# Kernel optimization log

Measured on AMD Instinct MI355X. Metric: run time of the kernel, lower is better.

The kernel has to match this reference:

```python
import jax, jax.numpy as jnp
import numpy as np

EPS = 1e-8
K_KNN = 20

def vn_lin(W, x):
    # W: [Cout, Cin], x: [B, Cin, 3, ...] -> [B, Cout, 3, ...]
    return jnp.einsum('oi,bi...->bo...', W, x)

def vn_relu(Wd, x):
    # VNLeakyReLU with negative_slope=0, share_nonlinearity=False
    d = jnp.einsum('oi,bi...->bo...', Wd, x)
    dot = jnp.sum(x * d, axis=2, keepdims=True)   # sum over 3-vector axis
    dsq = jnp.sum(d * d, axis=2, keepdims=True) + EPS
    return jnp.where(dot >= 0, x, x - (dot / dsq) * d)

def graph_feature_cross(p, k):
    # p: [B, N, 3] -> feat: [B, 3, 3, N, k]
    xx = jnp.sum(p * p, axis=-1)                       # [B,N]
    inner = jnp.einsum('bnd,bmd->bnm', p, p)           # [B,N,N]
    neg_dist = 2.0 * inner - xx[:, :, None] - xx[:, None, :]
    idx = jax.lax.top_k(neg_dist, k)[1]                # [B,N,k] nearest neighbors
    nbrs = jax.vmap(lambda pb, ib: pb[ib])(p, idx)     # [B,N,k,3]
    xr = jnp.broadcast_to(p[:, :, None, :], nbrs.shape)
    cross = jnp.cross(nbrs, xr)                        # [B,N,k,3]
    feat = jnp.stack([nbrs - xr, xr, cross], axis=3)   # [B,N,k,3(ch),3(vec)]
    return jnp.transpose(feat, (0, 3, 4, 1, 2))        # [B,3,3,N,k]

def setup_inputs() -> dict:
    key = jax.random.key(0)
    ks = jax.random.split(key, 9)
    B, N = 4, 2048
    H = 128           # hidden_dim // 3
    C_IN = 2 * H      # 256
    CC = 128          # c_dim // 3
    s_in = 1.0 / np.sqrt(C_IN)
    s_h = 1.0 / np.sqrt(H)
    return {
        'p': jax.random.normal(ks[0], (B, N, 3), dtype=jnp.float32),
        'fc_pos_W': jax.random.normal(ks[1], (C_IN, 3), dtype=jnp.float32) / np.sqrt(3.0),
        'blk_d0': jax.random.normal(ks[2], (5, C_IN, C_IN), dtype=jnp.float32) * s_in,
        'blk_W0': jax.random.normal(ks[3], (5, H, C_IN), dtype=jnp.float32) * s_in,
        'blk_d1': jax.random.normal(ks[4], (5, H, H), dtype=jnp.float32) * s_h,
        'blk_W1': jax.random.normal(ks[5], (5, H, H), dtype=jnp.float32) * s_h,
        'blk_Ws': jax.random.normal(ks[6], (5, H, C_IN), dtype=jnp.float32) * s_in,
        'fc_c_W': jax.random.normal(ks[7], (CC, H), dtype=jnp.float32) * s_h,
        'act_d': jax.random.normal(ks[8], (H, H), dtype=jnp.float32) * s_h,
    }

def reference(p, fc_pos_W, blk_d0, blk_W0, blk_d1, blk_W1, blk_Ws, fc_c_W, act_d):
    feat = graph_feature_cross(p, K_KNN)          # [B,3,3,N,k]
    x = vn_lin(fc_pos_W, feat)                    # [B,256,3,N,k]
    net = jnp.mean(x, axis=-1)                    # mean_pool over k -> [B,256,3,N]

    def block(i, x):
        h = vn_lin(blk_W0[i], vn_relu(blk_d0[i], x))
        dx = vn_lin(blk_W1[i], vn_relu(blk_d1[i], h))
        return vn_lin(blk_Ws[i], x) + dx          # shortcut (size_in != size_out)

    net = block(0, net)                           # [B,128,3,N]
    for i in range(1, 5):
        pooled = jnp.broadcast_to(jnp.mean(net, axis=3, keepdims=True), net.shape)
        net = block(i, jnp.concatenate([net, pooled], axis=1))
    net = jnp.mean(net, axis=3)                   # [B,128,3]
    c = vn_lin(fc_c_W, vn_relu(act_d, net))       # [B,128,3]
    return c.reshape(c.shape[0], -1)              # [B,384]
```

## Files before the change

### kernel.cpp

```cpp
#include <hip/hip_runtime.h>
#include <math.h>

#define N_PTS 2048
#define K_NN  20
#define K_D   10
#define WTOT  819200

typedef unsigned short u16;
typedef unsigned int   u32;
typedef _Float16 f16;
using half8   = __attribute__((ext_vector_type(8))) _Float16;
using floatx4 = __attribute__((ext_vector_type(4))) float;

__device__ __forceinline__ void split2h(float v, f16& h, f16& l) {
    h = (f16)v;
    l = (f16)((v - (float)h) * 1024.0f);
}

__device__ __forceinline__ float neg_dist(float4 q2, float4 c) {
    return fmaf(q2.x, c.x, fmaf(q2.y, c.y, fmaf(q2.z, c.z, -q2.w))) - c.w;
}

__global__ __launch_bounds__(256) void prep_kernel(
    const float* __restrict__ pts, float* __restrict__ m_out,
    const float* __restrict__ bd0, const float* __restrict__ bW0,
    const float* __restrict__ bd1, const float* __restrict__ bW1,
    const float* __restrict__ bWs, u16* __restrict__ Wswz,
    float* __restrict__ nm_acc)
{
    __shared__ float4 sp[N_PTS];
    if (blockIdx.x >= 1024) {
        int i = (blockIdx.x - 1024) * 256 + threadIdx.x;
        if (i >= WTOT) return;
        if (i < 7680) nm_acc[i] = 0.f;
        float v; int base, K, local;
        if (i < 327680)      { int rel = i;          base = (rel/65536)*65536;            local = rel%65536; K = 256; v = bd0[rel]; }
        else if (i < 491520) { int rel = i - 327680; base = 327680 + (rel/32768)*32768;   local = rel%32768; K = 256; v = bW0[rel]; }
        else if (i < 573440) { int rel = i - 491520; base = 491520 + (rel/16384)*16384;   local = rel%16384; K = 128; v = bd1[rel]; }
        else if (i < 655360) { int rel = i - 573440; base = 573440 + (rel/16384)*16384;   local = rel%16384; K = 128; v = bW1[rel]; }
        else                 { int rel = i - 655360; base = 655360 + (rel/32768)*32768;   local = rel%32768; K = 256; v = bWs[rel]; }
        int m = local / K, k = local % K;
        int NKF = K >> 5;
        int mf = m >> 4, r = m & 15;
        int kf = k >> 5, q = (k >> 3) & 3, ii = k & 7;
        int lane = q*16 + r;
        int dst = base + ((mf*NKF + kf)*64 + lane)*8 + ii;
        f16 h, l; split2h(v, h, l);
        f16* W = (f16*)Wswz;
        W[dst] = h; W[WTOT + dst] = l;
        return;
    }

    const int b     = blockIdx.x >> 8;
    const int qbase = (blockIdx.x & 255) << 3;
    const int ql    = threadIdx.x >> 5;
    const int sl    = threadIdx.x & 31;
    const float* pb = pts + (size_t)b * N_PTS * 3;
    for (int i = threadIdx.x; i < N_PTS; i += 256) {
        float x = pb[i*3+0], y = pb[i*3+1], z = pb[i*3+2];
        sp[i] = make_float4(x, y, z, x*x + y*y + z*z);
    }
    __syncthreads();

    const int n = qbase + ql;
    const float4 q = sp[n];
    const float4 q2 = make_float4(2.f*q.x, 2.f*q.y, 2.f*q.z, q.w);

    float t[K_D];
#pragma unroll
    for (int s = 0; s < K_D; ++s) t[s] = -INFINITY;

    for (int j = 0; j < N_PTS/32; ++j) {
        float4 c = sp[j*32 + sl];
        float v = neg_dist(q2, c);
#pragma unroll
        for (int s = 0; s < K_D; ++s) {
            float nx = (s < K_D-1) ? t[s+1] : INFINITY;
            t[s] = fminf(fmaxf(t[s], v), nx);
        }
    }

    float head = t[K_D-1];
    float T = -INFINITY;
#pragma unroll 1
    for (int e = 0; e < K_NN; ++e) {
        float v = head; int w = sl;
#pragma unroll
        for (int off = 1; off < 32; off <<= 1) {
            float vo = __shfl_xor(v, off);
            int   wo = __shfl_xor(w, off);
            bool take = (vo > v) || (vo == v && wo < w);
            v = take ? vo : v;
            w = take ? wo : w;
        }
        T = v;
        if (w == sl) {
#pragma unroll
            for (int s = K_D-1; s > 0; --s) t[s] = t[s-1];
            t[0] = -INFINITY;
            head = t[K_D-1];
        }
    }

    float sx = 0.f, sy = 0.f, sz = 0.f;
    for (int j = 0; j < N_PTS/32; ++j) {
        float4 c = sp[j*32 + sl];
        float v = neg_dist(q2, c);
        if (v >= T) { sx += c.x; sy += c.y; sz += c.z; }
    }
#pragma unroll
    for (int off = 1; off < 32; off <<= 1) {
        sx += __shfl_xor(sx, off);
        sy += __shfl_xor(sy, off);
        sz += __shfl_xor(sz, off);
    }
    if (sl == 0) {
        const float inv = 1.0f / (float)K_NN;
        const int pt = b * N_PTS + n;
        m_out[pt*3+0] = sx * inv;
        m_out[pt*3+1] = sy * inv;
        m_out[pt*3+2] = sz * inv;
    }
}

template<int MF, int JF>
__device__ __forceinline__ void run_gemm_hi(
    const f16* __restrict__ Whi, size_t aoff,
    int NK, const f16* Blds, int bstride, int lane,
    floatx4 (&acc)[MF][JF])
{
    const int l15 = lane & 15;
    const int lq8 = (lane >> 4) * 8;
    half8 Aa[MF], Ab[MF];

    auto loada = [&](half8 (&dst)[MF], int kf) {
#pragma unroll
        for (int fm = 0; fm < MF; ++fm)
            dst[fm] = *(const half8*)(Whi + aoff + (size_t)(fm*NK + kf)*512 + (size_t)lane*8);
    };
    auto step = [&](half8 (&af)[MF], int kf) {
        half8 bq[JF];
#pragma unroll
        for (int fj = 0; fj < JF; ++fj)
            bq[fj] = *(const half8*)&Blds[(fj*16 + l15)*bstride + kf*32 + lq8];
#pragma unroll
        for (int fm = 0; fm < MF; ++fm)
#pragma unroll
            for (int fj = 0; fj < JF; ++fj)
                acc[fm][fj] = __builtin_amdgcn_mfma_f32_16x16x32_f16(af[fm], bq[fj], acc[fm][fj], 0, 0, 0);
    };

    loada(Aa, 0);
#pragma unroll 1
    for (int kf = 0; kf < NK; kf += 2) {
        loada(Ab, kf + 1);
        step(Aa, kf);
        if (kf + 2 < NK) loada(Aa, kf + 2);
        step(Ab, kf + 1);
    }
}

template<int MF, int JF>
__device__ __forceinline__ void run_gemm_split(
    const f16* __restrict__ Whi, const f16* __restrict__ Wlo, size_t aoff,
    int NK, const f16* Blds, int bstride, int lane,
    floatx4 (&acc)[MF][JF], floatx4 (&accL)[MF][JF])
{
    const int l15 = lane & 15;
    const int lq8 = (lane >> 4) * 8;
    half8 Aa[2*MF], Ab[2*MF];

    auto loada = [&](half8 (&dst)[2*MF], int kf) {
#pragma unroll
        for (int fm = 0; fm < MF; ++fm) {
            size_t fo = aoff + (size_t)(fm*NK + kf)*512 + (size_t)lane*8;
            dst[fm*2+0] = *(const half8*)(Whi + fo);
            dst[fm*2+1] = *(const half8*)(Wlo + fo);
        }
    };
    auto step = [&](half8 (&af)[2*MF], int kf) {
        half8 bq[JF];
#pragma unroll
        for (int fj = 0; fj < JF; ++fj)
            bq[fj] = *(const half8*)&Blds[(fj*16 + l15)*bstride + kf*32 + lq8];
#pragma unroll
        for (int fm = 0; fm < MF; ++fm)
#pragma unroll
            for (int fj = 0; fj < JF; ++fj) {
                acc[fm][fj]  = __builtin_amdgcn_mfma_f32_16x16x32_f16(af[fm*2+0], bq[fj], acc[fm][fj], 0, 0, 0);
                accL[fm][fj] = __builtin_amdgcn_mfma_f32_16x16x32_f16(af[fm*2+1], bq[fj], accL[fm][fj], 0, 0, 0);
            }
    };

    loada(Aa, 0);
#pragma unroll 1
    for (int kf = 0; kf < NK; kf += 2) {
        loada(Ab, kf + 1);
        step(Aa, kf);
        if (kf + 2 < NK) loada(Aa, kf + 2);
        step(Ab, kf + 1);
    }
}

__device__ __forceinline__ uint2 pack_res(floatx4 a, floatx4 aL) {
    u16 hh[4];
#pragma unroll
    for (int r = 0; r < 4; ++r) {
        f16 hv = (f16)(a[r] + aL[r] * (1.0f/1024.0f));
        hh[r] = *(u16*)&hv;
    }
    uint2 pv;
    pv.x = (u32)hh[0] | ((u32)hh[1] << 16);
    pv.y = (u32)hh[2] | ((u32)hh[3] << 16);
    return pv;
}

__device__ __forceinline__ uint2 pack_hi(floatx4 a) {
    u16 hh[4];
#pragma unroll
    for (int r = 0; r < 4; ++r) {
        f16 hv = (f16)a[r];
        hh[r] = *(u16*)&hv;
    }
    uint2 pv;
    pv.x = (u32)hh[0] | ((u32)hh[1] << 16);
    pv.y = (u32)hh[2] | ((u32)hh[3] << 16);
    return pv;
}

__global__ __launch_bounds__(256, 3) void resblk_kernel(
    const u16* __restrict__ Wswz,
    int offD0, int offW0, int offD1, int offW1, int offWs,
    const f16* __restrict__ netIn, const float* __restrict__ nm_prev,
    const float* __restrict__ pts, const float* __restrict__ m_buf,
    const float* __restrict__ fcW,
    f16* __restrict__ netOut, float* __restrict__ nm_out, int blk0,
    int skip_store)
{
    __shared__ struct {
        f16 X[48*264];
        union { f16 d[48*264]; float C[48*132]; } Y;
    } s;

    const int tid  = threadIdx.x;
    const int jb   = blockIdx.x * 48;
    const int bB   = blockIdx.x >> 7;
    const int lane = tid & 63;
    const int wv   = tid >> 6;
    const f16* Whi = (const f16*)Wswz;
    const f16* Wlo = Whi + WTOT;

    if (blk0) {
        float* Hf = (float*)s.Y.C;
        const int ptbase = blockIdx.x * 16;
        for (int i = tid; i < 768; i += 256) Hf[i] = fcW[i];
        if (tid < 96) Hf[768 + tid] = (tid < 48) ? pts[ptbase*3 + tid]
                                                 : m_buf[ptbase*3 + tid - 48];
        __syncthreads();
#pragma unroll 1
        for (int it = 0; it < 6; ++it) {
            int idx = tid + 256*it;
            int r = idx >> 5;
            int cg = idx & 31;
            int l = r / 3, v = r - l*3;
            float pv0[3] = {Hf[768+l*3], Hf[768+l*3+1], Hf[768+l*3+2]};
            float mv0[3] = {Hf[816+l*3], Hf[816+l*3+1], Hf[816+l*3+2]};
            int v1 = (v==2) ? 0 : v+1;
            int v2 = (v==0) ? 2 : v-1;
            float av = mv0[v] - pv0[v];
            float bv = pv0[v];
            float cv = mv0[v1]*pv0[v2] - mv0[v2]*pv0[v1];
            half8 o;
#pragma unroll
            for (int k = 0; k < 8; ++k) {
                int ch = cg*8 + k;
                o[k] = (f16)(Hf[ch*3+0]*av + Hf[ch*3+1]*bv + Hf[ch*3+2]*cv);
            }
            *(half8*)&s.X[r*264 + cg*8] = o;
        }
    } else {
#pragma unroll 1
        for (int it = 0; it < 6; ++it) {
            int idx = tid + 256*it;
            int r = idx >> 5;
            int cg = idx & 31;
            if (cg < 16) {
                uint4 vv = *(const uint4*)(netIn + (size_t)(jb + r)*128 + cg*8);
                *(uint4*)&s.X[r*264 + cg*8] = vv;
            } else {
                int v = r % 3;
                const float* np = nm_prev + (bB*3+v)*128 + (cg-16)*8;
                half8 o;
#pragma unroll
                for (int k = 0; k < 8; ++k) o[k] = (f16)(np[k] * (1.0f/2048.0f));
                *(half8*)&s.X[r*264 + cg*8] = o;
            }
        }
    }
    __syncthreads();

    floatx4 acc4[2][3], accL4[2][3];
#pragma unroll
    for (int a = 0; a < 2; ++a)
#pragma unroll
        for (int b = 0; b < 3; ++b) { acc4[a][b] = (floatx4){0,0,0,0}; accL4[a][b] = (floatx4){0,0,0,0}; }

    {
        floatx4 acc[4][3];
#pragma unroll
        for (int a = 0; a < 4; ++a)
#pragma unroll
            for (int b = 0; b < 3; ++b) acc[a][b] = (floatx4){0,0,0,0};
        run_gemm_hi<4,3>(Whi, (size_t)offD0 + (size_t)wv*16384, 8, s.X, 264, lane, acc);
#pragma unroll
        for (int fm = 0; fm < 4; ++fm)
#pragma unroll
            for (int fj = 0; fj < 3; ++fj) {
                int mloc = wv*64 + fm*16 + (lane>>4)*4;
                int jl   = fj*16 + (lane & 15);
                *(uint2*)&s.Y.d[jl*264 + mloc] = pack_hi(acc[fm][fj]);
            }
    }
    __syncthreads();

    run_gemm_split<2,3>(Whi, Wlo, (size_t)offWs + (size_t)wv*8192, 8, s.X, 264, lane, acc4, accL4);

#pragma unroll 1
    for (int it = 0; it < 2; ++it) {
        int idx = tid + 256*it;
        int l = idx >> 5, cg = idx & 31;
        half8 xa = *(const half8*)&s.X[(l*3+0)*264 + cg*8];
        half8 xb = *(const half8*)&s.X[(l*3+1)*264 + cg*8];
        half8 xc = *(const half8*)&s.X[(l*3+2)*264 + cg*8];
        half8 da = *(const half8*)&s.Y.d[(l*3+0)*264 + cg*8];
        half8 db = *(const half8*)&s.Y.d[(l*3+1)*264 + cg*8];
        half8 dc = *(const half8*)&s.Y.d[(l*3+2)*264 + cg*8];
        half8 ya, yb, yc;
#pragma unroll
        for (int k = 0; k < 8; ++k) {
            float x0 = (float)xa[k], x1 = (float)xb[k], x2 = (float)xc[k];
            float d0 = (float)da[k], d1 = (float)db[k], d2 = (float)dc[k];
            float dot = x0*d0 + x1*d1 + x2*d2;
            float y0, y1, y2;
            if (dot >= 0.f) { y0 = x0; y1 = x1; y2 = x2; }
            else {
                float dsq = d0*d0 + d1*d1 + d2*d2 + 1e-8f;
                float sc = dot / dsq;
                y0 = x0 - sc*d0; y1 = x1 - sc*d1; y2 = x2 - sc*d2;
            }
            ya[k] = (f16)y0; yb[k] = (f16)y1; yc[k] = (f16)y2;
        }
        *(half8*)&s.Y.d[(l*3+0)*264 + cg*8] = ya;
        *(half8*)&s.Y.d[(l*3+1)*264 + cg*8] = yb;
        *(half8*)&s.Y.d[(l*3+2)*264 + cg*8] = yc;
    }
    __syncthreads();

    {
        floatx4 acc[2][3], accL[2][3];
#pragma unroll
        for (int a = 0; a < 2; ++a)
#pragma unroll
            for (int b = 0; b < 3; ++b) { acc[a][b] = (floatx4){0,0,0,0}; accL[a][b] = (floatx4){0,0,0,0}; }
        run_gemm_split<2,3>(Whi, Wlo, (size_t)offW0 + (size_t)wv*8192, 8, s.Y.d, 264, lane, acc, accL);
#pragma unroll
        for (int fm = 0; fm < 2; ++fm)
#pragma unroll
            for (int fj = 0; fj < 3; ++fj) {
                int mloc = wv*32 + fm*16 + (lane>>4)*4;
                int jl   = fj*16 + (lane & 15);
                *(uint2*)&s.X[jl*136 + mloc] = pack_res(acc[fm][fj], accL[fm][fj]);
            }
    }
    __syncthreads();

    {
        floatx4 acc[2][3];
#pragma unroll
        for (int a = 0; a < 2; ++a)
#pragma unroll
            for (int b = 0; b < 3; ++b) acc[a][b] = (floatx4){0,0,0,0};
        run_gemm_hi<2,3>(Whi, (size_t)offD1 + (size_t)wv*4096, 4, s.X, 136, lane, acc);
#pragma unroll
        for (int fm = 0; fm < 2; ++fm)
#pragma unroll
            for (int fj = 0; fj < 3; ++fj) {
                int mloc = wv*32 + fm*16 + (lane>>4)*4;
                int jl   = fj*16 + (lane & 15);
                *(uint2*)&s.Y.d[jl*136 + mloc] = pack_hi(acc[fm][fj]);
            }
    }
    __syncthreads();

    {
        int l = tid >> 4, cg = tid & 15;
        half8 xa = *(const half8*)&s.X[(l*3+0)*136 + cg*8];
        half8 xb = *(const half8*)&s.X[(l*3+1)*136 + cg*8];
        half8 xc = *(const half8*)&s.X[(l*3+2)*136 + cg*8];
        half8 da = *(const half8*)&s.Y.d[(l*3+0)*136 + cg*8];
        half8 db = *(const half8*)&s.Y.d[(l*3+1)*136 + cg*8];
        half8 dc = *(const half8*)&s.Y.d[(l*3+2)*136 + cg*8];
        half8 ya, yb, yc;
#pragma unroll
        for (int k = 0; k < 8; ++k) {
            float x0 = (float)xa[k], x1 = (float)xb[k], x2 = (float)xc[k];
            float d0 = (float)da[k], d1 = (float)db[k], d2 = (float)dc[k];
            float dot = x0*d0 + x1*d1 + x2*d2;
            float y0, y1, y2;
            if (dot >= 0.f) { y0 = x0; y1 = x1; y2 = x2; }
            else {
                float dsq = d0*d0 + d1*d1 + d2*d2 + 1e-8f;
                float sc = dot / dsq;
                y0 = x0 - sc*d0; y1 = x1 - sc*d1; y2 = x2 - sc*d2;
            }
            ya[k] = (f16)y0; yb[k] = (f16)y1; yc[k] = (f16)y2;
        }
        __syncthreads();
        *(half8*)&s.X[(l*3+0)*136 + cg*8] = ya;
        *(half8*)&s.X[(l*3+1)*136 + cg*8] = yb;
        *(half8*)&s.X[(l*3+2)*136 + cg*8] = yc;
    }
    __syncthreads();

    run_gemm_split<2,3>(Whi, Wlo, (size_t)offW1 + (size_t)wv*4096, 4, s.X, 136, lane, acc4, accL4);

#pragma unroll
    for (int fm = 0; fm < 2; ++fm)
#pragma unroll
        for (int fj = 0; fj < 3; ++fj) {
            int mloc = wv*32 + fm*16 + (lane>>4)*4;
            int jl   = fj*16 + (lane & 15);
            floatx4 res;
#pragma unroll
            for (int r = 0; r < 4; ++r) res[r] = acc4[fm][fj][r] + accL4[fm][fj][r] * (1.0f/1024.0f);
            if (!skip_store) {
                u16 hh[4];
#pragma unroll
                for (int r = 0; r < 4; ++r) { f16 hv = (f16)res[r]; hh[r] = *(u16*)&hv; }
                uint2 pv;
                pv.x = (u32)hh[0] | ((u32)hh[1] << 16);
                pv.y = (u32)hh[2] | ((u32)hh[3] << 16);
                *(uint2*)(netOut + (size_t)(jb + jl)*128 + mloc) = pv;
            }
            *(floatx4*)&s.Y.C[jl*132 + mloc] = res;
        }
    __syncthreads();

#pragma unroll 1
    for (int idx = tid; idx < 384; idx += 256) {
        int v = idx >> 7, ch = idx & 127;
        float sum = 0.f;
#pragma unroll 1
        for (int pt = 0; pt < 16; ++pt) sum += s.Y.C[(pt*3+v)*132 + ch];
        atomicAdd(nm_out + (bB*3+v)*128 + ch, sum);
    }
}

__global__ __launch_bounds__(128) void final_kernel(const float* __restrict__ nm_sum,
                                                    const float* __restrict__ act_d,
                                                    const float* __restrict__ fc_c,
                                                    float* __restrict__ out)
{
    const int b = blockIdx.x;
    const int c = threadIdx.x;
    __shared__ float xs[128][3];
    __shared__ float ys[128][3];
    xs[c][0] = nm_sum[(b*3+0)*128 + c] * (1.0f/2048.0f);
    xs[c][1] = nm_sum[(b*3+1)*128 + c] * (1.0f/2048.0f);
    xs[c][2] = nm_sum[(b*3+2)*128 + c] * (1.0f/2048.0f);
    __syncthreads();
    float d0 = 0.f, d1 = 0.f, d2 = 0.f;
    for (int i = 0; i < 128; ++i) {
        float w = act_d[c*128 + i];
        d0 = fmaf(w, xs[i][0], d0);
        d1 = fmaf(w, xs[i][1], d1);
        d2 = fmaf(w, xs[i][2], d2);
    }
    float x0 = xs[c][0], x1 = xs[c][1], x2 = xs[c][2];
    float dot = x0*d0 + x1*d1 + x2*d2;
    float y0, y1, y2;
    if (dot >= 0.f) { y0 = x0; y1 = x1; y2 = x2; }
    else {
        float dsq = d0*d0 + d1*d1 + d2*d2 + 1e-8f;
        float sc = dot / dsq;
        y0 = x0 - sc*d0; y1 = x1 - sc*d1; y2 = x2 - sc*d2;
    }
    ys[c][0] = y0; ys[c][1] = y1; ys[c][2] = y2;
    __syncthreads();
    float o0 = 0.f, o1 = 0.f, o2 = 0.f;
    for (int i = 0; i < 128; ++i) {
        float w = fc_c[c*128 + i];
        o0 = fmaf(w, ys[i][0], o0);
        o1 = fmaf(w, ys[i][1], o1);
        o2 = fmaf(w, ys[i][2], o2);
    }
    out[b*384 + c*3 + 0] = o0;
    out[b*384 + c*3 + 1] = o1;
    out[b*384 + c*3 + 2] = o2;
}

extern "C" void kernel_launch(void* const* d_in, const int* in_sizes, int n_in,
                              void* d_out, int out_size, void* d_ws, size_t ws_size,
                              hipStream_t stream)
{
    const float* p      = (const float*)d_in[0];
    const float* fc_pos = (const float*)d_in[1];
    const float* bd0    = (const float*)d_in[2];
    const float* bW0    = (const float*)d_in[3];
    const float* bd1    = (const float*)d_in[4];
    const float* bW1    = (const float*)d_in[5];
    const float* bWs    = (const float*)d_in[6];
    const float* fc_c   = (const float*)d_in[7];
    const float* act_d  = (const float*)d_in[8];
    float* out = (float*)d_out;

    char* w = (char*)d_ws;
    float* m_buf  = (float*)w;  w += 98304;
    float* nm_acc = (float*)w;  w += 5*1536*4;
    u16*   Wswz   = (u16*)w;    w += (size_t)2*WTOT*2;
    f16*   netA   = (f16*)w;    w += (size_t)24576*128*2;
    f16*   netB   = (f16*)w;    w += (size_t)24576*128*2;

    prep_kernel<<<dim3(1024 + 3200), dim3(256), 0, stream>>>(
        p, m_buf, bd0, bW0, bd1, bW1, bWs, Wswz, nm_acc);

    f16* nIn = netA;
    f16* nOut = netB;
    for (int blk = 0; blk < 5; ++blk) {
        const int offD0 = blk*65536;
        const int offW0 = 327680 + blk*32768;
        const int offD1 = 491520 + blk*16384;
        const int offW1 = 573440 + blk*16384;
        const int offWs = 655360 + blk*32768;
        const float* nmp = (blk == 0) ? nullptr : (nm_acc + (blk-1)*1536);
        resblk_kernel<<<dim3(512), dim3(256), 0, stream>>>(
            Wswz, offD0, offW0, offD1, offW1, offWs,
            (blk == 0) ? netA : nIn, nmp, p, m_buf, fc_pos,
            nOut, nm_acc + blk*1536, (blk == 0) ? 1 : 0,
            (blk == 4) ? 1 : 0);
        f16* tmp = nIn; nIn = nOut; nOut = tmp;
    }

    final_kernel<<<dim3(4), dim3(128), 0, stream>>>(nm_acc + 4*1536, act_d, fc_c, out);

    (void)in_sizes; (void)n_in; (void)out_size; (void)ws_size;
}
```

Baseline: 242.2 us.

## Fuse residual blocks and final head into one persistent kernel with atomic barriers

```diff
diff --git a/kernel.cpp b/kernel.cpp
--- a/kernel.cpp
+++ b/kernel.cpp
@@ -5,6 +5,9 @@
 #define K_NN  20
 #define K_D   10
 #define WTOT  819200
+#define NM_REP 8
+#define NM_STRIDE 1536
+#define NM_BLK (NM_REP*NM_STRIDE)
 
 typedef unsigned short u16;
 typedef unsigned int   u32;
@@ -32,7 +35,7 @@
     if (blockIdx.x >= 1024) {
         int i = (blockIdx.x - 1024) * 256 + threadIdx.x;
         if (i >= WTOT) return;
-        if (i < 7680) nm_acc[i] = 0.f;
+        if (i < 5*NM_BLK + 32) nm_acc[i] = 0.f;
         float v; int base, K, local;
         if (i < 327680)      { int rel = i;          base = (rel/65536)*65536;            local = rel%65536; K = 256; v = bd0[rel]; }
         else if (i < 491520) { int rel = i - 327680; base = 327680 + (rel/32768)*32768;   local = rel%32768; K = 256; v = bW0[rel]; }
@@ -228,14 +231,13 @@
     return pv;
 }
 
-__global__ __launch_bounds__(256, 3) void resblk_kernel(
+__global__ __launch_bounds__(256, 3) void resnet_kernel(
     const u16* __restrict__ Wswz,
-    int offD0, int offW0, int offD1, int offW1, int offWs,
-    const f16* __restrict__ netIn, const float* __restrict__ nm_prev,
     const float* __restrict__ pts, const float* __restrict__ m_buf,
     const float* __restrict__ fcW,
-    f16* __restrict__ netOut, float* __restrict__ nm_out, int blk0,
-    int skip_store)
+    float* __restrict__ nm_acc, int* __restrict__ cnt,
+    const float* __restrict__ act_d, const float* __restrict__ fc_c,
+    float* __restrict__ out)
 {
     __shared__ struct {
         f16 X[48*264];
@@ -243,103 +245,270 @@
     } s;
 
     const int tid  = threadIdx.x;
-    const int jb   = blockIdx.x * 48;
     const int bB   = blockIdx.x >> 7;
     const int lane = tid & 63;
     const int wv   = tid >> 6;
     const f16* Whi = (const f16*)Wswz;
     const f16* Wlo = Whi + WTOT;
 
-    if (blk0) {
-        float* Hf = (float*)s.Y.C;
-        const int ptbase = blockIdx.x * 16;
-        for (int i = tid; i < 768; i += 256) Hf[i] = fcW[i];
-        if (tid < 96) Hf[768 + tid] = (tid < 48) ? pts[ptbase*3 + tid]
-                                                 : m_buf[ptbase*3 + tid - 48];
-        __syncthreads();
-#pragma unroll 1
-        for (int it = 0; it < 6; ++it) {
+#pragma unroll 1
+    for (int st = 0; st < 5; ++st) {
+        const int offD0 = st*65536;
+        const int offW0 = 327680 + st*32768;
+        const int offD1 = 491520 + st*16384;
+        const int offW1 = 573440 + st*16384;
+        const int offWs = 655360 + st*32768;
+
+        if (st == 0) {
+            float* Hf = (float*)s.Y.C;
+            const int ptbase = blockIdx.x * 16;
+            for (int i = tid; i < 768; i += 256) Hf[i] = fcW[i];
+            if (tid < 96) Hf[768 + tid] = (tid < 48) ? pts[ptbase*3 + tid]
+                                                     : m_buf[ptbase*3 + tid - 48];
+            __syncthreads();
+#pragma unroll 1
+            for (int it = 0; it < 6; ++it) {
+                int idx = tid + 256*it;
+                int r = idx >> 5;
+                int cg = idx & 31;
+                int l = r / 3, v = r - l*3;
+                float pv0[3] = {Hf[768+l*3], Hf[768+l*3+1], Hf[768+l*3+2]};
+                float mv0[3] = {Hf[816+l*3], Hf[816+l*3+1], Hf[816+l*3+2]};
+                int v1 = (v==2) ? 0 : v+1;
+                int v2 = (v==0) ? 2 : v-1;
+                float av = mv0[v] - pv0[v];
+                float bv = pv0[v];
+                float cv = mv0[v1]*pv0[v2] - mv0[v2]*pv0[v1];
+                half8 o;
+#pragma unroll
+                for (int k = 0; k < 8; ++k) {
+                    int ch = cg*8 + k;
+                    o[k] = (f16)(Hf[ch*3+0]*av + Hf[ch*3+1]*bv + Hf[ch*3+2]*cv);
+                }
+                *(half8*)&s.X[r*264 + cg*8] = o;
+            }
+            __syncthreads();
+        }
+
+        floatx4 acc4[2][3], accL4[2][3];
+#pragma unroll
+        for (int a = 0; a < 2; ++a)
+#pragma unroll
+            for (int b = 0; b < 3; ++b) { acc4[a][b] = (floatx4){0,0,0,0}; accL4[a][b] = (floatx4){0,0,0,0}; }
+
+        {
+            floatx4 acc[4][3];
+#pragma unroll
+            for (int a = 0; a < 4; ++a)
+#pragma unroll
+                for (int b = 0; b < 3; ++b) acc[a][b] = (floatx4){0,0,0,0};
+            run_gemm_hi<4,3>(Whi, (size_t)offD0 + (size_t)wv*16384, 8, s.X, 264, lane, acc);
+#pragma unroll
+            for (int fm = 0; fm < 4; ++fm)
+#pragma unroll
+                for (int fj = 0; fj < 3; ++fj) {
+                    int mloc = wv*64 + fm*16 + (lane>>4)*4;
+                    int jl   = fj*16 + (lane & 15);
+                    *(uint2*)&s.Y.d[jl*264 + mloc] = pack_hi(acc[fm][fj]);
+                }
+        }
+        __syncthreads();
+
+        run_gemm_split<2,3>(Whi, Wlo, (size_t)offWs + (size_t)wv*8192, 8, s.X, 264, lane, acc4, accL4);
+
+#pragma unroll 1
+        for (int it = 0; it < 2; ++it) {
             int idx = tid + 256*it;
-            int r = idx >> 5;
-            int cg = idx & 31;
-            int l = r / 3, v = r - l*3;
-            float pv0[3] = {Hf[768+l*3], Hf[768+l*3+1], Hf[768+l*3+2]};
-            float mv0[3] = {Hf[816+l*3], Hf[816+l*3+1], Hf[816+l*3+2]};
-            int v1 = (v==2) ? 0 : v+1;
-            int v2 = (v==0) ? 2 : v-1;
-            float av = mv0[v] - pv0[v];
-            float bv = pv0[v];
-            float cv = mv0[v1]*pv0[v2] - mv0[v2]*pv0[v1];
-            half8 o;
+            int l = idx >> 5, cg = idx & 31;
+            half8 xa = *(const half8*)&s.X[(l*3+0)*264 + cg*8];
+            half8 xb = *(const half8*)&s.X[(l*3+1)*264 + cg*8];
+            half8 xc = *(const half8*)&s.X[(l*3+2)*264 + cg*8];
+            half8 da = *(const half8*)&s.Y.d[(l*3+0)*264 + cg*8];
+            half8 db = *(const half8*)&s.Y.d[(l*3+1)*264 + cg*8];
+            half8 dc = *(const half8*)&s.Y.d[(l*3+2)*264 + cg*8];
+            half8 ya, yb, yc;
 #pragma unroll
             for (int k = 0; k < 8; ++k) {
-                int ch = cg*8 + k;
-                o[k] = (f16)(Hf[ch*3+0]*av + Hf[ch*3+1]*bv + Hf[ch*3+2]*cv);
-            }
-            *(half8*)&s.X[r*264 + cg*8] = o;
-        }
-    } else {
-#pragma unroll 1
-        for (int it = 0; it < 6; ++it) {
+                float x0 = (float)xa[k], x1 = (float)xb[k], x2 = (float)xc[k];
+                float d0 = (float)da[k], d1 = (float)db[k], d2 = (float)dc[k];
+                float dot = x0*d0 + x1*d1 + x2*d2;
+                float y0, y1, y2;
+                if (dot >= 0.f) { y0 = x0; y1 = x1; y2 = x2; }
+                else {
+                    float dsq = d0*d0 + d1*d1 + d2*d2 + 1e-8f;
+                    float sc = dot / dsq;
+                    y0 = x0 - sc*d0; y1 = x1 - sc*d1; y2 = x2 - sc*d2;
+                }
+                ya[k] = (f16)y0; yb[k] = (f16)y1; yc[k] = (f16)y2;
+            }
+            *(half8*)&s.Y.d[(l*3+0)*264 + cg*8] = ya;
+            *(half8*)&s.Y.d[(l*3+1)*264 + cg*8] = yb;
+            *(half8*)&s.Y.d[(l*3+2)*264 + cg*8] = yc;
+        }
+        __syncthreads();
+
+        {
+            floatx4 acc[2][3], accL[2][3];
+#pragma unroll
+            for (int a = 0; a < 2; ++a)
+#pragma unroll
+                for (int b = 0; b < 3; ++b) { acc[a][b] = (floatx4){0,0,0,0}; accL[a][b] = (floatx4){0,0,0,0}; }
+            run_gemm_split<2,3>(Whi, Wlo, (size_t)offW0 + (size_t)wv*8192, 8, s.Y.d, 264, lane, acc, accL);
+#pragma unroll
+            for (int fm = 0; fm < 2; ++fm)
+#pragma unroll
+                for (int fj = 0; fj < 3; ++fj) {
+                    int mloc = wv*32 + fm*16 + (lane>>4)*4;
+                    int jl   = fj*16 + (lane & 15);
+                    *(uint2*)&s.X[jl*136 + mloc] = pack_res(acc[fm][fj], accL[fm][fj]);
+                }
+        }
+        __syncthreads();
+
+        {
+            floatx4 acc[2][3];
+#pragma unroll
+            for (int a = 0; a < 2; ++a)
+#pragma unroll
+                for (int b = 0; b < 3; ++b) acc[a][b] = (floatx4){0,0,0,0};
+            run_gemm_hi<2,3>(Whi, (size_t)offD1 + (size_t)wv*4096, 4, s.X, 136, lane, acc);
+#pragma unroll
+            for (int fm = 0; fm < 2; ++fm)
+#pragma unroll
+                for (int fj = 0; fj < 3; ++fj) {
+                    int mloc = wv*32 + fm*16 + (lane>>4)*4;
+                    int jl   = fj*16 + (lane & 15);
+                    *(uint2*)&s.Y.d[jl*136 + mloc] = pack_hi(acc[fm][fj]);
+                }
+        }
+        __syncthreads();
+
+        {
+            int l = tid >> 4, cg = tid & 15;
+            half8 xa = *(const half8*)&s.X[(l*3+0)*136 + cg*8];
+            half8 xb = *(const half8*)&s.X[(l*3+1)*136 + cg*8];
+            half8 xc = *(const half8*)&s.X[(l*3+2)*136 + cg*8];
+            half8 da = *(const half8*)&s.Y.d[(l*3+0)*136 + cg*8];
+            half8 db = *(const half8*)&s.Y.d[(l*3+1)*136 + cg*8];
+            half8 dc = *(const half8*)&s.Y.d[(l*3+2)*136 + cg*8];
+            half8 ya, yb, yc;
+#pragma unroll
+            for (int k = 0; k < 8; ++k) {
+                float x0 = (float)xa[k], x1 = (float)xb[k], x2 = (float)xc[k];
+                float d0 = (float)da[k], d1 = (float)db[k], d2 = (float)dc[k];
+                float dot = x0*d0 + x1*d1 + x2*d2;
+                float y0, y1, y2;
+                if (dot >= 0.f) { y0 = x0; y1 = x1; y2 = x2; }
+                else {
+                    float dsq = d0*d0 + d1*d1 + d2*d2 + 1e-8f;
+                    float sc = dot / dsq;
+                    y0 = x0 - sc*d0; y1 = x1 - sc*d1; y2 = x2 - sc*d2;
+                }
+                ya[k] = (f16)y0; yb[k] = (f16)y1; yc[k] = (f16)y2;
+            }
+            __syncthreads();
+            *(half8*)&s.X[(l*3+0)*136 + cg*8] = ya;
+            *(half8*)&s.X[(l*3+1)*136 + cg*8] = yb;
+            *(half8*)&s.X[(l*3+2)*136 + cg*8] = yc;
+        }
+        __syncthreads();
+
+        run_gemm_split<2,3>(Whi, Wlo, (size_t)offW1 + (size_t)wv*4096, 4, s.X, 136, lane, acc4, accL4);
+        __syncthreads();
+
+#pragma unroll
+        for (int fm = 0; fm < 2; ++fm)
+#pragma unroll
+            for (int fj = 0; fj < 3; ++fj) {
+                int mloc = wv*32 + fm*16 + (lane>>4)*4;
+                int jl   = fj*16 + (lane & 15);
+                floatx4 res;
+#pragma unroll
+                for (int r = 0; r < 4; ++r) res[r] = acc4[fm][fj][r] + accL4[fm][fj][r] * (1.0f/1024.0f);
+                *(uint2*)&s.X[jl*264 + mloc] = pack_res(acc4[fm][fj], accL4[fm][fj]);
+                *(floatx4*)&s.Y.C[jl*132 + mloc] = res;
+            }
+        __syncthreads();
+
+        const int rsel = (blockIdx.x & (NM_REP-1)) * NM_STRIDE;
+        float* nmS = nm_acc + (size_t)st*NM_BLK;
+#pragma unroll 1
+        for (int idx = tid; idx < 384; idx += 256) {
+            int v = idx >> 7, ch = idx & 127;
+            float sum = 0.f;
+#pragma unroll 1
+            for (int pt = 0; pt < 16; ++pt) sum += s.Y.C[(pt*3+v)*132 + ch];
+            atomicAdd(nmS + rsel + (bB*3+v)*128 + ch, sum);
+        }
+        __threadfence();
+        __syncthreads();
+        if (tid == 0)
+            __hip_atomic_fetch_add(&cnt[st*4+bB], 1, __ATOMIC_RELEASE, __HIP_MEMORY_SCOPE_AGENT);
+        if (st == 4) break;
+
+        if (tid == 0) {
+            while (__hip_atomic_load(&cnt[st*4+bB], __ATOMIC_ACQUIRE, __HIP_MEMORY_SCOPE_AGENT) < 128)
+                __builtin_amdgcn_s_sleep(2);
+        }
+        __syncthreads();
+
+        f16* nmT = (f16*)&s.Y;
+#pragma unroll 1
+        for (int idx = tid; idx < 384; idx += 256) {
+            int v = idx >> 7, ch = idx & 127;
+            float sum = 0.f;
+#pragma unroll
+            for (int rep = 0; rep < NM_REP; ++rep)
+                sum += __hip_atomic_load(nmS + rep*NM_STRIDE + (bB*3+v)*128 + ch,
+                                         __ATOMIC_RELAXED, __HIP_MEMORY_SCOPE_AGENT);
+            nmT[idx] = (f16)(sum * (1.0f/2048.0f));
+        }
+        __syncthreads();
+#pragma unroll
+        for (int it = 0; it < 3; ++it) {
             int idx = tid + 256*it;
-            int r = idx >> 5;
-            int cg = idx & 31;
-            if (cg < 16) {
-                uint4 vv = *(const uint4*)(netIn + (size_t)(jb + r)*128 + cg*8);
-                *(uint4*)&s.X[r*264 + cg*8] = vv;
-            } else {
-                int v = r % 3;
-                const float* np = nm_prev + (bB*3+v)*128 + (cg-16)*8;
-                half8 o;
-#pragma unroll
-                for (int k = 0; k < 8; ++k) o[k] = (f16)(np[k] * (1.0f/2048.0f));
-                *(half8*)&s.X[r*264 + cg*8] = o;
-            }
-        }
-    }
-    __syncthreads();
-
-    floatx4 acc4[2][3], accL4[2][3];
-#pragma unroll
-    for (int a = 0; a < 2; ++a)
-#pragma unroll
-        for (int b = 0; b < 3; ++b) { acc4[a][b] = (floatx4){0,0,0,0}; accL4[a][b] = (floatx4){0,0,0,0}; }
-
-    {
-        floatx4 acc[4][3];
-#pragma unroll
-        for (int a = 0; a < 4; ++a)
-#pragma unroll
-            for (int b = 0; b < 3; ++b) acc[a][b] = (floatx4){0,0,0,0};
-        run_gemm_hi<4,3>(Whi, (size_t)offD0 + (size_t)wv*16384, 8, s.X, 264, lane, acc);
-#pragma unroll
-        for (int fm = 0; fm < 4; ++fm)
-#pragma unroll
-            for (int fj = 0; fj < 3; ++fj) {
-                int mloc = wv*64 + fm*16 + (lane>>4)*4;
-                int jl   = fj*16 + (lane & 15);
-                *(uint2*)&s.Y.d[jl*264 + mloc] = pack_hi(acc[fm][fj]);
-            }
-    }
-    __syncthreads();
-
-    run_gemm_split<2,3>(Whi, Wlo, (size_t)offWs + (size_t)wv*8192, 8, s.X, 264, lane, acc4, accL4);
-
-#pragma unroll 1
-    for (int it = 0; it < 2; ++it) {
-        int idx = tid + 256*it;
-        int l = idx >> 5, cg = idx & 31;
-        half8 xa = *(const half8*)&s.X[(l*3+0)*264 + cg*8];
-        half8 xb = *(const half8*)&s.X[(l*3+1)*264 + cg*8];
-        half8 xc = *(const half8*)&s.X[(l*3+2)*264 + cg*8];
-        half8 da = *(const half8*)&s.Y.d[(l*3+0)*264 + cg*8];
-        half8 db = *(const half8*)&s.Y.d[(l*3+1)*264 + cg*8];
-        half8 dc = *(const half8*)&s.Y.d[(l*3+2)*264 + cg*8];
-        half8 ya, yb, yc;
-#pragma unroll
-        for (int k = 0; k < 8; ++k) {
-            float x0 = (float)xa[k], x1 = (float)xb[k], x2 = (float)xc[k];
-            float d0 = (float)da[k], d1 = (float)db[k], d2 = (float)dc[k];
+            int r = idx >> 4;
+            int cg = (idx & 15) + 16;
+            int v = r % 3;
+            *(half8*)&s.X[r*264 + cg*8] = *(const half8*)&nmT[v*128 + (cg-16)*8];
+        }
+        __syncthreads();
+    }
+
+    if (blockIdx.x < 4) {
+        const int b = blockIdx.x;
+        if (tid == 0) {
+            while (__hip_atomic_load(&cnt[16+b], __ATOMIC_ACQUIRE, __HIP_MEMORY_SCOPE_AGENT) < 128)
+                __builtin_amdgcn_s_sleep(2);
+        }
+        __syncthreads();
+        float* xs = (float*)&s;
+        float* ys = xs + 384;
+        const float* nm4 = nm_acc + (size_t)4*NM_BLK;
+        if (tid < 128) {
+            int c = tid;
+            float s0 = 0.f, s1 = 0.f, s2 = 0.f;
+#pragma unroll
+            for (int rep = 0; rep < NM_REP; ++rep) {
+                s0 += __hip_atomic_load(nm4 + rep*NM_STRIDE + (b*3+0)*128 + c, __ATOMIC_RELAXED, __HIP_MEMORY_SCOPE_AGENT);
+                s1 += __hip_atomic_load(nm4 + rep*NM_STRIDE + (b*3+1)*128 + c, __ATOMIC_RELAXED, __HIP_MEMORY_SCOPE_AGENT);
+                s2 += __hip_atomic_load(nm4 + rep*NM_STRIDE + (b*3+2)*128 + c, __ATOMIC_RELAXED, __HIP_MEMORY_SCOPE_AGENT);
+            }
+            xs[c*3+0] = s0 * (1.0f/2048.0f);
+            xs[c*3+1] = s1 * (1.0f/2048.0f);
+            xs[c*3+2] = s2 * (1.0f/2048.0f);
+        }
+        __syncthreads();
+        if (tid < 128) {
+            int c = tid;
+            float d0 = 0.f, d1 = 0.f, d2 = 0.f;
+            for (int i = 0; i < 128; ++i) {
+                float w = act_d[c*128 + i];
+                d0 = fmaf(w, xs[i*3+0], d0);
+                d1 = fmaf(w, xs[i*3+1], d1);
+                d2 = fmaf(w, xs[i*3+2], d2);
+            }
+            float x0 = xs[c*3+0], x1 = xs[c*3+1], x2 = xs[c*3+2];
             float dot = x0*d0 + x1*d1 + x2*d2;
             float y0, y1, y2;
             if (dot >= 0.f) { y0 = x0; y1 = x1; y2 = x2; }
@@ -348,155 +517,23 @@
                 float sc = dot / dsq;
                 y0 = x0 - sc*d0; y1 = x1 - sc*d1; y2 = x2 - sc*d2;
             }
-            ya[k] = (f16)y0; yb[k] = (f16)y1; yc[k] = (f16)y2;
-        }
-        *(half8*)&s.Y.d[(l*3+0)*264 + cg*8] = ya;
-        *(half8*)&s.Y.d[(l*3+1)*264 + cg*8] = yb;
-        *(half8*)&s.Y.d[(l*3+2)*264 + cg*8] = yc;
-    }
-    __syncthreads();
-
-    {
-        floatx4 acc[2][3], accL[2][3];
-#pragma unroll
-        for (int a = 0; a < 2; ++a)
-#pragma unroll
-            for (int b = 0; b < 3; ++b) { acc[a][b] = (floatx4){0,0,0,0}; accL[a][b] = (floatx4){0,0,0,0}; }
-        run_gemm_split<2,3>(Whi, Wlo, (size_t)offW0 + (size_t)wv*8192, 8, s.Y.d, 264, lane, acc, accL);
-#pragma unroll
-        for (int fm = 0; fm < 2; ++fm)
-#pragma unroll
-            for (int fj = 0; fj < 3; ++fj) {
-                int mloc = wv*32 + fm*16 + (lane>>4)*4;
-                int jl   = fj*16 + (lane & 15);
-                *(uint2*)&s.X[jl*136 + mloc] = pack_res(acc[fm][fj], accL[fm][fj]);
-            }
-    }
-    __syncthreads();
-
-    {
-        floatx4 acc[2][3];
-#pragma unroll
-        for (int a = 0; a < 2; ++a)
-#pragma unroll
-            for (int b = 0; b < 3; ++b) acc[a][b] = (floatx4){0,0,0,0};
-        run_gemm_hi<2,3>(Whi, (size_t)offD1 + (size_t)wv*4096, 4, s.X, 136, lane, acc);
-#pragma unroll
-        for (int fm = 0; fm < 2; ++fm)
-#pragma unroll
-            for (int fj = 0; fj < 3; ++fj) {
-                int mloc = wv*32 + fm*16 + (lane>>4)*4;
-                int jl   = fj*16 + (lane & 15);
-                *(uint2*)&s.Y.d[jl*136 + mloc] = pack_hi(acc[fm][fj]);
-            }
-    }
-    __syncthreads();
-
-    {
-        int l = tid >> 4, cg = tid & 15;
-        half8 xa = *(const half8*)&s.X[(l*3+0)*136 + cg*8];
-        half8 xb = *(const half8*)&s.X[(l*3+1)*136 + cg*8];
-        half8 xc = *(const half8*)&s.X[(l*3+2)*136 + cg*8];
-        half8 da = *(const half8*)&s.Y.d[(l*3+0)*136 + cg*8];
-        half8 db = *(const half8*)&s.Y.d[(l*3+1)*136 + cg*8];
-        half8 dc = *(const half8*)&s.Y.d[(l*3+2)*136 + cg*8];
-        half8 ya, yb, yc;
-#pragma unroll
-        for (int k = 0; k < 8; ++k) {
-            float x0 = (float)xa[k], x1 = (float)xb[k], x2 = (float)xc[k];
-            float d0 = (float)da[k], d1 = (float)db[k], d2 = (float)dc[k];
-            float dot = x0*d0 + x1*d1 + x2*d2;
-            float y0, y1, y2;
-            if (dot >= 0.f) { y0 = x0; y1 = x1; y2 = x2; }
-            else {
-                float dsq = d0*d0 + d1*d1 + d2*d2 + 1e-8f;
-                float sc = dot / dsq;
-                y0 = x0 - sc*d0; y1 = x1 - sc*d1; y2 = x2 - sc*d2;
-            }
-            ya[k] = (f16)y0; yb[k] = (f16)y1; yc[k] = (f16)y2;
-        }
-        __syncthreads();
-        *(half8*)&s.X[(l*3+0)*136 + cg*8] = ya;
-        *(half8*)&s.X[(l*3+1)*136 + cg*8] = yb;
-        *(half8*)&s.X[(l*3+2)*136 + cg*8] = yc;
-    }
-    __syncthreads();
-
-    run_gemm_split<2,3>(Whi, Wlo, (size_t)offW1 + (size_t)wv*4096, 4, s.X, 136, lane, acc4, accL4);
-
-#pragma unroll
-    for (int fm = 0; fm < 2; ++fm)
-#pragma unroll
-        for (int fj = 0; fj < 3; ++fj) {
-            int mloc = wv*32 + fm*16 + (lane>>4)*4;
-            int jl   = fj*16 + (lane & 15);
-            floatx4 res;
-#pragma unroll
-            for (int r = 0; r < 4; ++r) res[r] = acc4[fm][fj][r] + accL4[fm][fj][r] * (1.0f/1024.0f);
-            if (!skip_store) {
-                u16 hh[4];
-#pragma unroll
-                for (int r = 0; r < 4; ++r) { f16 hv = (f16)res[r]; hh[r] = *(u16*)&hv; }
-                uint2 pv;
-                pv.x = (u32)hh[0] | ((u32)hh[1] << 16);
-                pv.y = (u32)hh[2] | ((u32)hh[3] << 16);
-                *(uint2*)(netOut + (size_t)(jb + jl)*128 + mloc) = pv;
-            }
-            *(floatx4*)&s.Y.C[jl*132 + mloc] = res;
-        }
-    __syncthreads();
-
-#pragma unroll 1
-    for (int idx = tid; idx < 384; idx += 256) {
-        int v = idx >> 7, ch = idx & 127;
-        float sum = 0.f;
-#pragma unroll 1
-        for (int pt = 0; pt < 16; ++pt) sum += s.Y.C[(pt*3+v)*132 + ch];
-        atomicAdd(nm_out + (bB*3+v)*128 + ch, sum);
-    }
-}
-
-__global__ __launch_bounds__(128) void final_kernel(const float* __restrict__ nm_sum,
-                                                    const float* __restrict__ act_d,
-                                                    const float* __restrict__ fc_c,
-                                                    float* __restrict__ out)
-{
-    const int b = blockIdx.x;
-    const int c = threadIdx.x;
-    __shared__ float xs[128][3];
-    __shared__ float ys[128][3];
-    xs[c][0] = nm_sum[(b*3+0)*128 + c] * (1.0f/2048.0f);
-    xs[c][1] = nm_sum[(b*3+1)*128 + c] * (1.0f/2048.0f);
-    xs[c][2] = nm_sum[(b*3+2)*128 + c] * (1.0f/2048.0f);
-    __syncthreads();
-    float d0 = 0.f, d1 = 0.f, d2 = 0.f;
-    for (int i = 0; i < 128; ++i) {
-        float w = act_d[c*128 + i];
-        d0 = fmaf(w, xs[i][0], d0);
-        d1 = fmaf(w, xs[i][1], d1);
-        d2 = fmaf(w, xs[i][2], d2);
-    }
-    float x0 = xs[c][0], x1 = xs[c][1], x2 = xs[c][2];
-    float dot = x0*d0 + x1*d1 + x2*d2;
-    float y0, y1, y2;
-    if (dot >= 0.f) { y0 = x0; y1 = x1; y2 = x2; }
-    else {
-        float dsq = d0*d0 + d1*d1 + d2*d2 + 1e-8f;
-        float sc = dot / dsq;
-        y0 = x0 - sc*d0; y1 = x1 - sc*d1; y2 = x2 - sc*d2;
-    }
-    ys[c][0] = y0; ys[c][1] = y1; ys[c][2] = y2;
-    __syncthreads();
-    float o0 = 0.f, o1 = 0.f, o2 = 0.f;
-    for (int i = 0; i < 128; ++i) {
-        float w = fc_c[c*128 + i];
-        o0 = fmaf(w, ys[i][0], o0);
-        o1 = fmaf(w, ys[i][1], o1);
-        o2 = fmaf(w, ys[i][2], o2);
-    }
-    out[b*384 + c*3 + 0] = o0;
-    out[b*384 + c*3 + 1] = o1;
-    out[b*384 + c*3 + 2] = o2;
+            ys[c*3+0] = y0; ys[c*3+1] = y1; ys[c*3+2] = y2;
+        }
+        __syncthreads();
+        if (tid < 128) {
+            int c = tid;
+            float o0 = 0.f, o1 = 0.f, o2 = 0.f;
+            for (int i = 0; i < 128; ++i) {
+                float w = fc_c[c*128 + i];
+                o0 = fmaf(w, ys[i*3+0], o0);
+                o1 = fmaf(w, ys[i*3+1], o1);
+                o2 = fmaf(w, ys[i*3+2], o2);
+            }
+            out[b*384 + c*3 + 0] = o0;
+            out[b*384 + c*3 + 1] = o1;
+            out[b*384 + c*3 + 2] = o2;
+        }
+    }
 }
 
 extern "C" void kernel_launch(void* const* d_in, const int* in_sizes, int n_in,
@@ -516,32 +553,15 @@
 
     char* w = (char*)d_ws;
     float* m_buf  = (float*)w;  w += 98304;
-    float* nm_acc = (float*)w;  w += 5*1536*4;
+    float* nm_acc = (float*)w;  w += (size_t)5*NM_BLK*4;
+    int*   cnt    = (int*)w;    w += 128;
     u16*   Wswz   = (u16*)w;    w += (size_t)2*WTOT*2;
-    f16*   netA   = (f16*)w;    w += (size_t)24576*128*2;
-    f16*   netB   = (f16*)w;    w += (size_t)24576*128*2;
 
     prep_kernel<<<dim3(1024 + 3200), dim3(256), 0, stream>>>(
         p, m_buf, bd0, bW0, bd1, bW1, bWs, Wswz, nm_acc);
 
-    f16* nIn = netA;
-    f16* nOut = netB;
-    for (int blk = 0; blk < 5; ++blk) {
-        const int offD0 = blk*65536;
-        const int offW0 = 327680 + blk*32768;
-        const int offD1 = 491520 + blk*16384;
-        const int offW1 = 573440 + blk*16384;
-        const int offWs = 655360 + blk*32768;
-        const float* nmp = (blk == 0) ? nullptr : (nm_acc + (blk-1)*1536);
-        resblk_kernel<<<dim3(512), dim3(256), 0, stream>>>(
-            Wswz, offD0, offW0, offD1, offW1, offWs,
-            (blk == 0) ? netA : nIn, nmp, p, m_buf, fc_pos,
-            nOut, nm_acc + blk*1536, (blk == 0) ? 1 : 0,
-            (blk == 4) ? 1 : 0);
-        f16* tmp = nIn; nIn = nOut; nOut = tmp;
-    }
-
-    final_kernel<<<dim3(4), dim3(128), 0, stream>>>(nm_acc + 4*1536, act_d, fc_c, out);
+    resnet_kernel<<<dim3(512), dim3(256), 0, stream>>>(
+        Wswz, p, m_buf, fc_pos, nm_acc, cnt, act_d, fc_c, out);
 
     (void)in_sizes; (void)n_in; (void)out_size; (void)ws_size;
 }
```

After: 541.5 us. 124% more time.
